# Optimization experiments

Hardware: AMD Instinct MI355X
Metric: run time of the kernel (lower is better)

Reference implementation:

```python
import jax, jax.numpy as jnp
import numpy as np

NUM_LAYERS = 3
H = 128          # hidden_dim
COMP_DIM = 128
PROT_DIM = 128
EPS = 1e-6


def setup_inputs() -> dict:
    key = jax.random.key(0)
    ks = jax.random.split(key, 20)
    B, Lc, Lp = 16, 512, 4096
    s = 0.05
    inp = {
        "comp_feat": jax.random.normal(ks[0], (B, Lc, COMP_DIM), jnp.float32),
        "comp_mask": jax.random.randint(ks[1], (B, Lc), 0, 2, jnp.int32),
        "prot_feat": jax.random.normal(ks[2], (B, Lp, PROT_DIM), jnp.float32),
        "prot_mask": jax.random.randint(ks[3], (B, Lp), 0, 2, jnp.int32),
        # per-layer params, stacked on leading layer axis. Linear(x) = x @ W + b
        # (W stored already transposed relative to torch's [out,in] layout).
        "Wc": jax.random.normal(ks[4], (NUM_LAYERS, COMP_DIM, H), jnp.float32) * s,
        "bc": jnp.zeros((NUM_LAYERS, H), jnp.float32),
        "Wp": jax.random.normal(ks[5], (NUM_LAYERS, PROT_DIM, H), jnp.float32) * s,
        "bp": jnp.zeros((NUM_LAYERS, H), jnp.float32),
        "Wbl": jax.random.normal(ks[6], (NUM_LAYERS, H, H), jnp.float32) * s,  # bilinear, no bias
        "Wac": jax.random.normal(ks[7], (NUM_LAYERS, H), jnp.float32) * s,    # Linear(H,1) weight
        "bac": jnp.zeros((NUM_LAYERS,), jnp.float32),
        "Wap": jax.random.normal(ks[8], (NUM_LAYERS, H), jnp.float32) * s,
        "bap": jnp.zeros((NUM_LAYERS,), jnp.float32),
        "Wcomb_c": jax.random.normal(ks[9], (NUM_LAYERS * H, H), jnp.float32) * s,
        "bcomb_c": jnp.zeros((H,), jnp.float32),
        "Wcomb_p": jax.random.normal(ks[10], (NUM_LAYERS * H, H), jnp.float32) * s,
        "bcomb_p": jnp.zeros((H,), jnp.float32),
    }
    return inp


def _masked_softmax(scores, mask):
    # faithful to torch: max over ALL entries (mask applied post-exp), +1e-6 denom
    m = jnp.max(scores, axis=-1, keepdims=True)
    e = jnp.exp(scores - m) * mask
    return e / (jnp.sum(e, axis=-1, keepdims=True) + EPS)


def reference(comp_feat, comp_mask, prot_feat, prot_mask,
              Wc, bc, Wp, bp, Wbl, Wac, bac, Wap, bap,
              Wcomb_c, bcomb_c, Wcomb_p, bcomb_p):
    cm = comp_mask.astype(jnp.float32)  # [B,Lc]
    pm = prot_mask.astype(jnp.float32)  # [B,Lp]
    comp_pooled_list, prot_pooled_list = [], []
    comp_context = prot_context = None
    for i in range(NUM_LAYERS):
        comp_proj = jnp.tanh(comp_feat @ Wc[i] + bc[i])   # [B,Lc,H]
        prot_proj = jnp.tanh(prot_feat @ Wp[i] + bp[i])   # [B,Lp,H]
        comp_bil = comp_proj @ Wbl[i]                      # [B,Lc,H]
        scores = jnp.einsum('bqh,bkh->bqk', comp_bil, prot_proj)  # [B,Lc,Lp]
        scores = scores * (cm[:, :, None] * pm[:, None, :])
        # broadcast-multiply-sum in torch == matmul; same math, efficient form
        comp_context = jnp.einsum('bqk,bkh->bqh', scores, prot_proj)  # [B,Lc,H]
        prot_context = jnp.einsum('bqk,bqh->bkh', scores, comp_proj)  # [B,Lp,H]
        cw = _masked_softmax(comp_context @ Wac[i] + bac[i], cm)  # [B,Lc]
        pw = _masked_softmax(prot_context @ Wap[i] + bap[i], pm)  # [B,Lp]
        comp_pooled_list.append(jnp.einsum('bqh,bq->bh', comp_proj, cw))
        prot_pooled_list.append(jnp.einsum('bkh,bk->bh', prot_proj, pw))
    comp_final = jnp.concatenate(comp_pooled_list, axis=1) @ Wcomb_c + bcomb_c
    prot_final = jnp.concatenate(prot_pooled_list, axis=1) @ Wcomb_p + bcomb_p
    # contexts returned are from the last layer (matches torch loop-variable leak)
    return (comp_final, prot_final, comp_context, prot_context)
```

## Files before the change

### kernel.cpp

```cpp
#include <hip/hip_runtime.h>
#include <math.h>

#define B_ 16
#define LC_ 512
#define LP_ 4096
#define H_ 128
#define HH_ (H_*H_)

typedef unsigned long long u64t;
typedef unsigned short u16t;
typedef __attribute__((ext_vector_type(8))) short bf16x8;
typedef __attribute__((ext_vector_type(4))) float f32x4;

__device__ __forceinline__ u16t f2bf(float f) {
    union { float f; unsigned u; } v; v.f = f;
    unsigned r = (v.u + 0x7FFFu + ((v.u >> 16) & 1u)) >> 16;
    return (u16t)r;
}
__device__ __forceinline__ float bf2f(u16t s) {
    union { unsigned u; float f; } v; v.u = ((unsigned)s) << 16; return v.f;
}
__device__ __forceinline__ float bflo(unsigned u) {
    union { unsigned u; float f; } v; v.u = u << 16; return v.f;
}
__device__ __forceinline__ float bfhi(unsigned u) {
    union { unsigned u; float f; } v; v.u = u & 0xffff0000u; return v.f;
}
__device__ __forceinline__ float ftanh(float x) {
    x = fminf(15.f, fmaxf(-15.f, x));
    float t = __expf(2.f * x);
    return (t - 1.f) / (t + 1.f);
}
__device__ __forceinline__ bf16x8 ldfragS(const short* base, int r, int k, int stride) {
    const u64t* p = (const u64t*)(base + (size_t)r * stride + k);
    union { bf16x8 v; u64t q[2]; } u;
    u.q[0] = p[0]; u.q[1] = p[1];
    return u.v;
}
__device__ __forceinline__ bf16x8 ldfragG(const u16t* p) {
    union { bf16x8 v; uint4 q; } u;
    u.q = *(const uint4*)p;
    return u.v;
}

__device__ __forceinline__ void wprep_body(const float* __restrict__ src,
                                           u16t* __restrict__ h, u16t* __restrict__ l,
                                           int t) {
    const int n = t >> 1, k0 = (t & 1) * 64;
#pragma unroll 4
    for (int k = 0; k < 64; ++k) {
        float v = src[(size_t)(k0 + k) * H_ + n];
        u16t hh = f2bf(v);
        h[(size_t)n * H_ + k0 + k] = hh;
        l[(size_t)n * H_ + k0 + k] = f2bf(v - bf2f(hh));
    }
}

__global__ __launch_bounds__(256) void prep_k(const float* __restrict__ s0,
                                              const float* __restrict__ s1,
                                              const float* __restrict__ s2,
                                              u16t* __restrict__ hi, u16t* __restrict__ lo,
                                              float* __restrict__ zcp,
                                              float* __restrict__ zout) {
    const int bid = blockIdx.x, t = threadIdx.x;
    if (bid < 9) {
        const int grp = bid / 3, lay = bid % 3;
        const float* src = (grp == 0 ? s0 : grp == 1 ? s1 : s2) + (size_t)lay * HH_;
        wprep_body(src, hi + (size_t)bid * HH_, lo + (size_t)bid * HH_, t);
    } else {
        float4 zero = make_float4(0.f, 0.f, 0.f, 0.f);
        float4* z = (float4*)zcp;
        for (int j = t; j < 3072; j += 256) z[j] = zero;
        float4* z2 = (float4*)zout;
        for (int j = t; j < 1024; j += 256) z2[j] = zero;
    }
}

__device__ __forceinline__ void stage_fp32(const float* __restrict__ X,
                                           short* __restrict__ Xs, int t) {
#pragma unroll
    for (int j = 0; j < 8; ++j) {
        int lin = j * 512 + t;
        int row = lin >> 5, c4 = lin & 31;
        float4 v = ((const float4*)X)[lin];
        u64t pk = (u64t)f2bf(v.x) | ((u64t)f2bf(v.y) << 16)
                | ((u64t)f2bf(v.z) << 32) | ((u64t)f2bf(v.w) << 48);
        *(u64t*)(Xs + (size_t)row * 136 + c4 * 4) = pk;
    }
}
__device__ __forceinline__ void stage_bf16(const u16t* __restrict__ X,
                                           short* __restrict__ Xs, int t) {
#pragma unroll
    for (int j = 0; j < 4; ++j) {
        int lin = j * 512 + t;
        *(uint4*)(Xs + (lin >> 4) * 136 + (lin & 15) * 8) = ((const uint4*)X)[lin];
    }
}

template<bool TANH, bool BF16OUT, bool LDSOUT>
__device__ __forceinline__ void gemm_core(const short* __restrict__ Xs,
                                          const u16t* __restrict__ Whi,
                                          const u16t* __restrict__ Wlo,
                                          const float* __restrict__ bias,
                                          const int* __restrict__ mrow,
                                          void* __restrict__ Yrow0,
                                          short* __restrict__ projLds, int t) {
    const int l = t & 63, w = t >> 6;
    const int lm = l & 15, lk = (l >> 4) * 8, lr = (l >> 4) * 4;
    const int wcol = w * 16;
    const size_t wrow = (size_t)(wcol + lm) * H_;
    f32x4 acc[8] = {};
#pragma unroll
    for (int ks = 0; ks < 128; ks += 32) {
        bf16x8 ah = ldfragG(Whi + wrow + ks + lk);
        bf16x8 al = ldfragG(Wlo + wrow + ks + lk);
#pragma unroll
        for (int rg = 0; rg < 8; ++rg) {
            bf16x8 xb = ldfragS(Xs, rg * 16 + lm, ks + lk, 136);
            acc[rg] = __builtin_amdgcn_mfma_f32_16x16x32_bf16(ah, xb, acc[rg], 0, 0, 0);
            acc[rg] = __builtin_amdgcn_mfma_f32_16x16x32_bf16(al, xb, acc[rg], 0, 0, 0);
        }
    }
    if (LDSOUT) __syncthreads();
    const int col = wcol + lr;
    float4 bq = make_float4(0.f, 0.f, 0.f, 0.f);
    if (bias) bq = *(const float4*)(bias + col);
#pragma unroll
    for (int rg = 0; rg < 8; ++rg) {
        const int row = rg * 16 + lm;
        float v0 = acc[rg][0] + bq.x, v1 = acc[rg][1] + bq.y;
        float v2 = acc[rg][2] + bq.z, v3 = acc[rg][3] + bq.w;
        if (TANH) { v0 = ftanh(v0); v1 = ftanh(v1); v2 = ftanh(v2); v3 = ftanh(v3); }
        if (mrow) {
            const float msc = (float)mrow[row];
            v0 *= msc; v1 *= msc; v2 *= msc; v3 *= msc;
        }
        if (BF16OUT) {
            u64t pk = (u64t)f2bf(v0) | ((u64t)f2bf(v1) << 16)
                    | ((u64t)f2bf(v2) << 32) | ((u64t)f2bf(v3) << 48);
            *(u64t*)((u16t*)Yrow0 + (size_t)row * H_ + col) = pk;
            if (LDSOUT) *(u64t*)(projLds + (size_t)row * 136 + col) = pk;
        } else {
            float4 o; o.x = v0; o.y = v1; o.z = v2; o.w = v3;
            *(float4*)((float*)Yrow0 + (size_t)row * H_ + col) = o;
        }
    }
}

__global__ __launch_bounds__(512) void gemmA_k(const float* __restrict__ prot_feat,
                                               const float* __restrict__ comp_feat,
                                               const u16t* __restrict__ WHi,
                                               const u16t* __restrict__ WLo,
                                               const float* __restrict__ bp,
                                               const float* __restrict__ bc,
                                               u16t* __restrict__ prot_proj,
                                               u16t* __restrict__ comp_proj,
                                               u16t* __restrict__ comp_bil) {
    __shared__ __align__(16) short Xs[128 * 136];
    const int t = threadIdx.x, z = blockIdx.z;
    if (z < 3) {
        const long row0 = (long)blockIdx.x * 128;
        stage_fp32(prot_feat + (size_t)row0 * H_, Xs, t);
        __syncthreads();
        gemm_core<true, true, false>(Xs, WHi + (size_t)z * HH_, WLo + (size_t)z * HH_,
            bp + z * H_, nullptr,
            prot_proj + ((size_t)z * B_ * LP_ + row0) * H_, nullptr, t);
    } else {
        if (blockIdx.x >= B_ * LC_ / 128) return;
        const int lay = z - 3;
        const long row0 = (long)blockIdx.x * 128;
        stage_fp32(comp_feat + (size_t)row0 * H_, Xs, t);
        __syncthreads();
        gemm_core<true, true, true>(Xs, WHi + (size_t)(3 + lay) * HH_, WLo + (size_t)(3 + lay) * HH_,
            bc + lay * H_, nullptr,
            comp_proj + ((size_t)lay * B_ * LC_ + row0) * H_, Xs, t);
        __syncthreads();
        gemm_core<false, true, false>(Xs, WHi + (size_t)(6 + lay) * HH_, WLo + (size_t)(6 + lay) * HH_,
            nullptr, nullptr,
            comp_bil + ((size_t)lay * B_ * LC_ + row0) * H_, nullptr, t);
    }
}

__device__ __forceinline__ void stage64_bf(const u16t* __restrict__ src,
                                           const int* __restrict__ maskrow,
                                           short* __restrict__ dst, int t) {
    const int m = t & 31, kq = t >> 5;
#pragma unroll
    for (int p = 0; p < 2; ++p) {
        const int kc = p * 32 + kq * 4;
        u64t q[4];
#pragma unroll
        for (int r = 0; r < 4; ++r) {
            u64t v = *(const u64t*)(src + (size_t)(kc + r) * H_ + m * 4);
            if (maskrow && !maskrow[kc + r]) v = 0;
            q[r] = v;
        }
#pragma unroll
        for (int i = 0; i < 4; ++i) {
            u64t val = ((q[0] >> (16 * i)) & 0xffffull)
                     | (((q[1] >> (16 * i)) & 0xffffull) << 16)
                     | (((q[2] >> (16 * i)) & 0xffffull) << 32)
                     | (((q[3] >> (16 * i)) & 0xffffull) << 48);
            *(u64t*)(dst + (size_t)(4 * m + i) * 68 + kc) = val;
        }
    }
}

__global__ __launch_bounds__(256) void syrkC_k(const u16t* __restrict__ prot_proj,
                                               const u16t* __restrict__ comp_bil,
                                               const u16t* __restrict__ comp_proj,
                                               const int* __restrict__ prot_mask,
                                               const int* __restrict__ comp_mask,
                                               float* __restrict__ partP,
                                               float* __restrict__ partC) {
    __shared__ __align__(16) short smem[2 * 128 * 68];
    const int t = threadIdx.x;
    const int slice = blockIdx.x, b = blockIdx.y, z = blockIdx.z;
    const bool isP = z < 3;
    const int lay = isP ? z : z - 3;
    const u16t* Xl = isP ? prot_proj : comp_bil;
    const u16t* Yr = isP ? prot_proj : comp_proj;
    const int* mask = isP ? prot_mask : comp_mask;
    const int Kb = isP ? LP_ : LC_;
    const int rps = Kb >> 3;
    float* part = isP ? partP : partC;
    short* Xt = smem;
    short* Yt = isP ? smem : smem + 128 * 68;

    const int l = t & 63, w = t >> 6;
    const int qi = (w >> 1) * 64, qj = (w & 1) * 64;
    const int lm = l & 15, lk = (l >> 4) * 8, lr = (l >> 4) * 4;
    f32x4 acc[4][4] = {};
    const int chunks = rps >> 6;
    const size_t doff = ((size_t)lay * B_ + b) * Kb;
    const size_t moff = (size_t)b * Kb;

    for (int c = 0; c < chunks; ++c) {
        const int kbase = slice * rps + c * 64;
        stage64_bf(Xl + (doff + kbase) * H_, mask + moff + kbase, Xt, t);
        if (!isP) stage64_bf(Yr + (doff + kbase) * H_, nullptr, Yt, t);
        __syncthreads();
#pragma unroll
        for (int ks = 0; ks < 64; ks += 32) {
            bf16x8 af[4], bfr[4];
#pragma unroll
            for (int it = 0; it < 4; ++it) af[it] = ldfragS(Xt, qi + it * 16 + lm, ks + lk, 68);
#pragma unroll
            for (int jt = 0; jt < 4; ++jt) bfr[jt] = ldfragS(Yt, qj + jt * 16 + lm, ks + lk, 68);
#pragma unroll
            for (int it = 0; it < 4; ++it)
#pragma unroll
                for (int jt = 0; jt < 4; ++jt)
                    acc[it][jt] = __builtin_amdgcn_mfma_f32_16x16x32_bf16(
                        af[it], bfr[jt], acc[it][jt], 0, 0, 0);
        }
        __syncthreads();
    }

    float* pb = part + (((size_t)lay * 8 + slice) * B_ + b) * HH_;
#pragma unroll
    for (int it = 0; it < 4; ++it)
#pragma unroll
        for (int jt = 0; jt < 4; ++jt)
#pragma unroll
            for (int r = 0; r < 4; ++r)
                pb[(size_t)(qi + it * 16 + lr + r) * H_ + qj + jt * 16 + lm] = acc[it][jt][r];
}

__global__ __launch_bounds__(256) void reduceC_k(const float4* __restrict__ partP,
                                                 const float4* __restrict__ partC,
                                                 const float* __restrict__ Wac,
                                                 const float* __restrict__ Wap,
                                                 float* __restrict__ vc, float* __restrict__ vp,
                                                 u16t* __restrict__ MNhi, u16t* __restrict__ MNlo) {
    const int lay = blockIdx.y, z = blockIdx.z, t = threadIdx.x;
    const size_t quarter = (size_t)B_ * HH_ / 4;
    const float4* p = (z ? partC : partP) + (size_t)lay * 8 * quarter;
    const size_t idx = (size_t)blockIdx.x * 256 + t;
    float4 a = p[idx];
#pragma unroll
    for (int s = 1; s < 8; ++s) {
        float4 v = p[(size_t)s * quarter + idx];
        a.x += v.x; a.y += v.y; a.z += v.z; a.w += v.w;
    }
    const int b = (int)(idx >> 12);
    const int q = (int)(idx & 4095);
    const int row = q >> 5, c4 = q & 31;

    const float* Wv = (z ? Wap : Wac) + lay * H_;
    float4 w4 = ((const float4*)Wv)[c4];
    float s = a.x * w4.x + a.y * w4.y + a.z * w4.z + a.w * w4.w;
#pragma unroll
    for (int o = 16; o > 0; o >>= 1) s += __shfl_down(s, o, 32);
    if ((t & 31) == 0)
        (z ? vp : vc)[((size_t)lay * B_ + b) * H_ + row] = s;

    if (lay == 2) {
        u16t* hi = MNhi + ((size_t)z * B_ + b) * HH_;
        u16t* lo = MNlo + ((size_t)z * B_ + b) * HH_;
        const int colb = c4 * 4;
        float av[4] = {a.x, a.y, a.z, a.w};
#pragma unroll
        for (int j = 0; j < 4; ++j) {
            u16t hh = f2bf(av[j]);
            hi[(size_t)(colb + j) * H_ + row] = hh;
            lo[(size_t)(colb + j) * H_ + row] = f2bf(av[j] - bf2f(hh));
        }
    }
}

__global__ __launch_bounds__(256) void logitsC_k(const u16t* __restrict__ prot_proj,
                                                 const u16t* __restrict__ comp_bil,
                                                 const int* __restrict__ prot_mask,
                                                 const int* __restrict__ comp_mask,
                                                 const float* __restrict__ vp,
                                                 const float* __restrict__ vc,
                                                 const float* __restrict__ bap,
                                                 const float* __restrict__ bac,
                                                 float* __restrict__ logp,
                                                 float* __restrict__ logc) {
    const int zz = blockIdx.z;
    const bool isP = zz < 3;
    if (!isP && blockIdx.x >= LC_ / 256) return;
    const int lay = isP ? zz : zz - 3;
    const int b = blockIdx.y, t = threadIdx.x;
    const int n = isP ? LP_ : LC_;
    __shared__ float v[H_];
    if (t < 128) v[t] = (isP ? vp : vc)[((size_t)lay * B_ + b) * H_ + t];
    __syncthreads();
    const int r = blockIdx.x * 256 + t;
    const u16t* feat = (isP ? prot_proj : comp_bil) + (((size_t)lay * B_ + b) * n + r) * H_;
    const uint2* f2 = (const uint2*)feat;
    const float4* v4 = (const float4*)v;
    float acc = 0.f;
#pragma unroll
    for (int h4 = 0; h4 < 32; ++h4) {
        uint2 u = f2[h4];
        float4 c = v4[h4];
        acc = fmaf(bflo(u.x), c.x, acc); acc = fmaf(bfhi(u.x), c.y, acc);
        acc = fmaf(bflo(u.y), c.z, acc); acc = fmaf(bfhi(u.y), c.w, acc);
    }
    const int mk = (isP ? prot_mask : comp_mask)[(size_t)b * n + r];
    (isP ? logp : logc)[((size_t)lay * B_ + b) * n + r] = (float)mk * acc + (isP ? bap : bac)[lay];
}

__global__ __launch_bounds__(256) void softmaxC_k(const float* __restrict__ logp,
                                                  const float* __restrict__ logc,
                                                  const int* __restrict__ prot_mask,
                                                  const int* __restrict__ comp_mask,
                                                  float* __restrict__ pw,
                                                  float* __restrict__ cw) {
    const int b = blockIdx.x, zz = blockIdx.y, t = threadIdx.x;
    const bool isP = zz < 3;
    const int lay = isP ? zz : zz - 3;
    const int n = isP ? LP_ : LC_;
    const float* l = (isP ? logp : logc) + ((size_t)lay * B_ + b) * n;
    const int* mk = (isP ? prot_mask : comp_mask) + (size_t)b * n;
    float* ww = (isP ? pw : cw) + ((size_t)lay * B_ + b) * n;
    __shared__ float Es[LP_];
    __shared__ float red[4];

    float mx = -1e30f;
    for (int q = t; q < n; q += 256) { float x = l[q]; Es[q] = x; mx = fmaxf(mx, x); }
#pragma unroll
    for (int o = 32; o > 0; o >>= 1) mx = fmaxf(mx, __shfl_down(mx, o, 64));
    if ((t & 63) == 0) red[t >> 6] = mx;
    __syncthreads();
    float m = fmaxf(fmaxf(red[0], red[1]), fmaxf(red[2], red[3]));
    __syncthreads();

    float s = 0.f;
    for (int q = t; q < n; q += 256) {
        float e = __expf(Es[q] - m) * (float)mk[q];
        Es[q] = e;
        s += e;
    }
#pragma unroll
    for (int o = 32; o > 0; o >>= 1) s += __shfl_down(s, o, 64);
    if ((t & 63) == 0) red[t >> 6] = s;
    __syncthreads();
    float denom = red[0] + red[1] + red[2] + red[3] + 1e-6f;
    for (int q = t; q < n; q += 256) ww[q] = Es[q] / denom;
}

__global__ __launch_bounds__(256) void poolC_k(const u16t* __restrict__ prot_proj,
                                               const u16t* __restrict__ comp_proj,
                                               const float* __restrict__ pw,
                                               const float* __restrict__ cw,
                                               float* __restrict__ pp, float* __restrict__ cp) {
    const int zz = blockIdx.z;
    const bool isP = zz < 3;
    if (!isP && blockIdx.y >= 4) return;
    const int lay = isP ? zz : zz - 3;
    const int n = isP ? LP_ : LC_;
    const int chunk = isP ? 256 : 128;
    const int b = blockIdx.x, t = threadIdx.x;
    const int th = t & 63, tq = t >> 6;
    const int q0 = blockIdx.y * chunk;
    const u16t* pb = (isP ? prot_proj : comp_proj) + (((size_t)lay * B_ + b) * n + q0) * H_;
    const float* wb = (isP ? pw : cw) + ((size_t)lay * B_ + b) * n + q0;
    float a0 = 0.f, a1 = 0.f;
    for (int q = tq; q < chunk; q += 4) {
        float wq = wb[q];
        unsigned u = *(const unsigned*)(pb + (size_t)q * H_ + th * 2);
        a0 = fmaf(bflo(u), wq, a0);
        a1 = fmaf(bfhi(u), wq, a1);
    }
    float* ob = (isP ? pp : cp) + ((size_t)lay * B_ + b) * H_;
    atomicAdd(&ob[th * 2], a0);
    atomicAdd(&ob[th * 2 + 1], a1);
}

__global__ __launch_bounds__(512) void ctxC_k(const u16t* __restrict__ comp_bil,
                                              const u16t* __restrict__ prot_proj,
                                              const u16t* __restrict__ MNhi,
                                              const u16t* __restrict__ MNlo,
                                              const int* __restrict__ comp_mask,
                                              const int* __restrict__ prot_mask,
                                              float* __restrict__ out_cc,
                                              float* __restrict__ out_pc) {
    __shared__ __align__(16) short Xs[128 * 136];
    const int t = threadIdx.x, z = blockIdx.z;
    const bool isC = z < 16;
    if (isC && blockIdx.x >= LC_ / 128) return;
    const int b = isC ? z : z - 16;
    const int n = isC ? LC_ : LP_;
    const size_t rowoff = (size_t)b * n + (size_t)blockIdx.x * 128;
    const u16t* X = (isC ? comp_bil + (size_t)2 * B_ * LC_ * H_
                         : prot_proj + (size_t)2 * B_ * LP_ * H_) + rowoff * H_;
    const u16t* Whi = MNhi + ((size_t)(isC ? 0 : 1) * B_ + b) * HH_;
    const u16t* Wlo = MNlo + ((size_t)(isC ? 0 : 1) * B_ + b) * HH_;
    const int* mrow = (isC ? comp_mask : prot_mask) + rowoff;
    float* Y = (isC ? out_cc : out_pc) + rowoff * H_;
    stage_bf16(X, Xs, t);
    __syncthreads();
    gemm_core<false, false, false>(Xs, Whi, Wlo, nullptr, mrow, Y, nullptr, t);
}

__global__ void finalC_k(const float* __restrict__ cp, const float* __restrict__ pp,
                         const float* __restrict__ Wcc, const float* __restrict__ bcc,
                         const float* __restrict__ Wcp, const float* __restrict__ bcp,
                         float* __restrict__ out_cf, float* __restrict__ out_pf) {
    const int z = blockIdx.z;
    const float* pooled = z ? pp : cp;
    const float* Wcomb = z ? Wcp : Wcc;
    const float* bcomb = z ? bcp : bcc;
    float* out = z ? out_pf : out_cf;
    const int b = blockIdx.x, h = threadIdx.x, j0 = blockIdx.y * 64;
    float acc = (blockIdx.y == 0) ? bcomb[h] : 0.f;
#pragma unroll 4
    for (int j = 0; j < 64; ++j) {
        int jj = j0 + j;
        int lay = jj >> 7, hh = jj & 127;
        acc = fmaf(pooled[((size_t)lay * B_ + b) * H_ + hh], Wcomb[(size_t)jj * H_ + h], acc);
    }
    atomicAdd(&out[b * H_ + h], acc);
}

extern "C" void kernel_launch(void* const* d_in, const int* in_sizes, int n_in,
                              void* d_out, int out_size, void* d_ws, size_t ws_size,
                              hipStream_t stream) {
    const float* comp_feat = (const float*)d_in[0];
    const int*   comp_mask = (const int*)d_in[1];
    const float* prot_feat = (const float*)d_in[2];
    const int*   prot_mask = (const int*)d_in[3];
    const float* Wc      = (const float*)d_in[4];
    const float* bc      = (const float*)d_in[5];
    const float* Wp      = (const float*)d_in[6];
    const float* bp      = (const float*)d_in[7];
    const float* Wbl     = (const float*)d_in[8];
    const float* Wac     = (const float*)d_in[9];
    const float* bac     = (const float*)d_in[10];
    const float* Wap     = (const float*)d_in[11];
    const float* bap     = (const float*)d_in[12];
    const float* Wcomb_c = (const float*)d_in[13];
    const float* bcomb_c = (const float*)d_in[14];
    const float* Wcomb_p = (const float*)d_in[15];
    const float* bcomb_p = (const float*)d_in[16];

    u16t* prot_proj = (u16t*)d_ws;
    u16t* comp_proj = prot_proj + (size_t)3 * B_ * LP_ * H_;
    u16t* comp_bil  = comp_proj + (size_t)3 * B_ * LC_ * H_;
    u16t* WHi  = comp_bil + (size_t)3 * B_ * LC_ * H_;
    u16t* WLo  = WHi + (size_t)9 * HH_;
    u16t* MNhi = WLo + (size_t)9 * HH_;
    u16t* MNlo = MNhi + (size_t)32 * HH_;
    float* f = (float*)(MNlo + (size_t)32 * HH_);
    float* vc = f;    f += (size_t)3 * B_ * H_;
    float* vp = f;    f += (size_t)3 * B_ * H_;
    float* logc = f;  f += (size_t)3 * B_ * LC_;
    float* logp = f;  f += (size_t)3 * B_ * LP_;
    float* cw = f;    f += (size_t)3 * B_ * LC_;
    float* pw = f;    f += (size_t)3 * B_ * LP_;
    float* cp = f;    f += 3 * B_ * H_;
    float* pp = f;    f += 3 * B_ * H_;
    float* partP = f + 0;
    partP = pp + 3 * B_ * H_;
    float* partC = partP + (size_t)3 * 8 * B_ * HH_;

    float* out_cf = (float*)d_out;
    float* out_pf = out_cf + B_ * H_;
    float* out_cc = out_pf + B_ * H_;
    float* out_pc = out_cc + (size_t)B_ * LC_ * H_;

    prep_k<<<dim3(10), 256, 0, stream>>>(Wp, Wc, Wbl, WHi, WLo, cp, out_cf);
    gemmA_k<<<dim3(B_ * LP_ / 128, 1, 6), 512, 0, stream>>>(
        prot_feat, comp_feat, WHi, WLo, bp, bc, prot_proj, comp_proj, comp_bil);
    syrkC_k<<<dim3(8, B_, 6), 256, 0, stream>>>(
        prot_proj, comp_bil, comp_proj, prot_mask, comp_mask, partP, partC);
    reduceC_k<<<dim3(256, 3, 2), 256, 0, stream>>>(
        (const float4*)partP, (const float4*)partC, Wac, Wap, vc, vp, MNhi, MNlo);
    logitsC_k<<<dim3(LP_ / 256, B_, 6), 256, 0, stream>>>(
        prot_proj, comp_bil, prot_mask, comp_mask, vp, vc, bap, bac, logp, logc);
    softmaxC_k<<<dim3(B_, 6), 256, 0, stream>>>(logp, logc, prot_mask, comp_mask, pw, cw);
    poolC_k<<<dim3(B_, 16, 6), 256, 0, stream>>>(prot_proj, comp_proj, pw, cw, pp, cp);
    ctxC_k<<<dim3(LP_ / 128, 1, 32), 512, 0, stream>>>(
        comp_bil, prot_proj, MNhi, MNlo, comp_mask, prot_mask, out_cc, out_pc);
    finalC_k<<<dim3(B_, 6, 2), 128, 0, stream>>>(
        cp, pp, Wcomb_c, bcomb_c, Wcomb_p, bcomb_p, out_cf, out_pf);
}
```

Before: 177.3 us.

## Stage input rows once and loop all three layers inside projection GEMM blocks

Replaces the per-layer z-dimension grid with one block per 128-row tile that stages the fp32 features into LDS once and then runs all three layers' projections from that staged tile. Comp blocks are placed first and use a second LDS buffer for the projected tile that feeds the bilinear GEMM. This removes the 3x redundant global reads and fp32→bf16 staging of the input features and drops the idle early-exit comp blocks. In exchange there are fewer, longer blocks, dynamic LDS doubles per block (likely reducing occupancy), and the three layers run serially inside each block.

```diff
diff --git a/kernel.cpp b/kernel.cpp
--- a/kernel.cpp
+++ b/kernel.cpp
@@ -147,7 +147,7 @@
     }
 }
 
-__global__ __launch_bounds__(512) void gemmA_k(const float* __restrict__ prot_feat,
+__global__ __launch_bounds__(512) void gemmB_k(const float* __restrict__ prot_feat,
                                                const float* __restrict__ comp_feat,
                                                const u16t* __restrict__ WHi,
                                                const u16t* __restrict__ WLo,
@@ -156,28 +156,33 @@
                                                u16t* __restrict__ prot_proj,
                                                u16t* __restrict__ comp_proj,
                                                u16t* __restrict__ comp_bil) {
-    __shared__ __align__(16) short Xs[128 * 136];
-    const int t = threadIdx.x, z = blockIdx.z;
-    if (z < 3) {
-        const long row0 = (long)blockIdx.x * 128;
+    extern __shared__ __align__(16) short smem[];
+    short* Xs = smem;
+    short* Ys = smem + 128 * 136;
+    const int t = threadIdx.x, bx = blockIdx.x;
+    if (bx < 64) {
+        const long row0 = (long)bx * 128;
+        stage_fp32(comp_feat + (size_t)row0 * H_, Xs, t);
+        __syncthreads();
+#pragma unroll 1
+        for (int lay = 0; lay < 3; ++lay) {
+            gemm_core<true, true, true>(Xs, WHi + (size_t)(3 + lay) * HH_,
+                WLo + (size_t)(3 + lay) * HH_, bc + lay * H_, nullptr,
+                comp_proj + ((size_t)lay * B_ * LC_ + row0) * H_, Ys, t);
+            __syncthreads();
+            gemm_core<false, true, false>(Ys, WHi + (size_t)(6 + lay) * HH_,
+                WLo + (size_t)(6 + lay) * HH_, nullptr, nullptr,
+                comp_bil + ((size_t)lay * B_ * LC_ + row0) * H_, nullptr, t);
+        }
+    } else {
+        const long row0 = (long)(bx - 64) * 128;
         stage_fp32(prot_feat + (size_t)row0 * H_, Xs, t);
         __syncthreads();
-        gemm_core<true, true, false>(Xs, WHi + (size_t)z * HH_, WLo + (size_t)z * HH_,
-            bp + z * H_, nullptr,
-            prot_proj + ((size_t)z * B_ * LP_ + row0) * H_, nullptr, t);
-    } else {
-        if (blockIdx.x >= B_ * LC_ / 128) return;
-        const int lay = z - 3;
-        const long row0 = (long)blockIdx.x * 128;
-        stage_fp32(comp_feat + (size_t)row0 * H_, Xs, t);
-        __syncthreads();
-        gemm_core<true, true, true>(Xs, WHi + (size_t)(3 + lay) * HH_, WLo + (size_t)(3 + lay) * HH_,
-            bc + lay * H_, nullptr,
-            comp_proj + ((size_t)lay * B_ * LC_ + row0) * H_, Xs, t);
-        __syncthreads();
-        gemm_core<false, true, false>(Xs, WHi + (size_t)(6 + lay) * HH_, WLo + (size_t)(6 + lay) * HH_,
-            nullptr, nullptr,
-            comp_bil + ((size_t)lay * B_ * LC_ + row0) * H_, nullptr, t);
+#pragma unroll 1
+        for (int lay = 0; lay < 3; ++lay)
+            gemm_core<true, true, false>(Xs, WHi + (size_t)lay * HH_,
+                WLo + (size_t)lay * HH_, bp + lay * H_, nullptr,
+                prot_proj + ((size_t)lay * B_ * LP_ + row0) * H_, nullptr, t);
     }
 }
 
@@ -494,8 +499,7 @@
     float* pw = f;    f += (size_t)3 * B_ * LP_;
     float* cp = f;    f += 3 * B_ * H_;
     float* pp = f;    f += 3 * B_ * H_;
-    float* partP = f + 0;
-    partP = pp + 3 * B_ * H_;
+    float* partP = pp + 3 * B_ * H_;
     float* partC = partP + (size_t)3 * 8 * B_ * HH_;
 
     float* out_cf = (float*)d_out;
@@ -504,7 +508,7 @@
     float* out_pc = out_cc + (size_t)B_ * LC_ * H_;
 
     prep_k<<<dim3(10), 256, 0, stream>>>(Wp, Wc, Wbl, WHi, WLo, cp, out_cf);
-    gemmA_k<<<dim3(B_ * LP_ / 128, 1, 6), 512, 0, stream>>>(
+    gemmB_k<<<dim3(64 + B_ * LP_ / 128), 512, 2 * 128 * 136 * sizeof(short), stream>>>(
         prot_feat, comp_feat, WHi, WLo, bp, bc, prot_proj, comp_proj, comp_bil);
     syrkC_k<<<dim3(8, B_, 6), 256, 0, stream>>>(
         prot_proj, comp_bil, comp_proj, prot_mask, comp_mask, partP, partC);
```

Result: no change. 179.6 us (+1.3%).
